# Optimization experiments

Hardware: AMD Instinct MI355X
Metric: run time of the kernel (lower is better)

## Reference

```python
import jax, jax.numpy as jnp
import numpy as np

N_NODES = 100000


def setup_inputs() -> dict:
    key = jax.random.key(0)
    ks = jax.random.split(key, 7)
    input_dim, hidden_dim = 64, 64
    x = jax.random.normal(ks[0], (N_NODES, input_dim), dtype=jnp.float32)
    edge_index = jax.random.randint(ks[1], (2, 1600000), 0, N_NODES, dtype=jnp.int64)
    weights = jax.random.uniform(ks[2], (N_NODES,), dtype=jnp.float32)
    # MLP params: Linear(input_dim->hidden), ReLU, Linear(hidden->hidden)
    s1 = 1.0 / np.sqrt(input_dim)
    s2 = 1.0 / np.sqrt(hidden_dim)
    W1 = jax.random.uniform(ks[3], (input_dim, hidden_dim), minval=-s1, maxval=s1, dtype=jnp.float32)
    b1 = jax.random.uniform(ks[4], (hidden_dim,), minval=-s1, maxval=s1, dtype=jnp.float32)
    W2 = jax.random.uniform(ks[5], (hidden_dim, hidden_dim), minval=-s2, maxval=s2, dtype=jnp.float32)
    b2 = jax.random.uniform(ks[6], (hidden_dim,), minval=-s2, maxval=s2, dtype=jnp.float32)
    return {"x": x, "edge_index": edge_index, "weights": weights,
            "W1": W1, "b1": b1, "W2": W2, "b2": b2}


def reference(x, edge_index, weights, W1, b1, W2, b2):
    src, dst = edge_index[0], edge_index[1]
    # GINConv (eps=0): h_i = MLP(x_i + sum_{j->i} x_j)
    agg = jax.ops.segment_sum(x[src], dst, num_segments=N_NODES)  # [N, d]
    h = agg + x
    h = jnp.maximum(h @ W1 + b1, 0.0)
    h = h @ W2 + b2                                                # [N, hidden]
    # per-node weighting then sum over nodes -> [1, 1, hidden]
    out = jnp.sum(h * weights[:, None], axis=0)
    return out[None, None, :]
```

## Files before the change

kernel.cpp:

```cpp
#include <hip/hip_runtime.h>
#include <hip/hip_bf16.h>

#define N_NODES 100000
#define N_EDGES 1600000
#define DIM 64
#define NB1 391
#define NGROUPS (N_NODES / 4)
#define NBLK_GM 1536
#define CSTRIDE 100096
#define E4 (N_EDGES / 4)
#define E4BLK 1563

#define OFF_COUNTS8 0
#define OFF_SOUT    800768
#define OFF_TOT     800848
#define OFF_OFFSETS 900944
#define OFF_BSUMS   1000960
#define OFF_CSR     1001472
#define OFF_RANK8   2601472
#define OFF_Y16     3001472

__device__ __forceinline__ float blo(unsigned u) { return __uint_as_float(u << 16); }
__device__ __forceinline__ float bhi(unsigned u) { return __uint_as_float(u & 0xffff0000u); }

__global__ __launch_bounds__(256) void convert_hist_kernel(
    const float* __restrict__ x, unsigned* __restrict__ y,
    const int* __restrict__ dst, int* __restrict__ counts8,
    unsigned* __restrict__ rank8)
{
    int i = blockIdx.x * 256 + threadIdx.x;
    if (i < N_NODES * DIM / 4) {
        float4 v = ((const float4*)x)[i];
        __hip_bfloat162 p0 = __float22bfloat162_rn(make_float2(v.x, v.y));
        __hip_bfloat162 p1 = __float22bfloat162_rn(make_float2(v.z, v.w));
        uint2 o;
        o.x = *reinterpret_cast<unsigned*>(&p0);
        o.y = *reinterpret_cast<unsigned*>(&p1);
        ((uint2*)y)[i] = o;
    }
    if (i < E4) {
        int4 d = ((const int4*)dst)[i];
        int* cnt = counts8 + (blockIdx.x & 7) * CSTRIDE;
        unsigned r0 = (unsigned)atomicAdd(&cnt[d.x], 1);
        unsigned r1 = (unsigned)atomicAdd(&cnt[d.y], 1);
        unsigned r2 = (unsigned)atomicAdd(&cnt[d.z], 1);
        unsigned r3 = (unsigned)atomicAdd(&cnt[d.w], 1);
        rank8[i] = r0 | (r1 << 8) | (r2 << 16) | (r3 << 24);
    }
}

__global__ __launch_bounds__(256) void colsum_blocksum_kernel(
    int* __restrict__ counts8, int* __restrict__ tot, int* __restrict__ bsums)
{
    __shared__ int s[256];
    int t = threadIdx.x;
    int idx = blockIdx.x * 256 + t;
    int run = 0;
    if (idx < N_NODES) {
        #pragma unroll
        for (int k = 0; k < 8; ++k) {
            int v = counts8[k * CSTRIDE + idx];
            counts8[k * CSTRIDE + idx] = run;
            run += v;
        }
        tot[idx] = run;
    }
    s[t] = (idx < N_NODES) ? run : 0;
    __syncthreads();
    for (int d = 128; d > 0; d >>= 1) {
        if (t < d) s[t] += s[t + d];
        __syncthreads();
    }
    if (t == 0) bsums[blockIdx.x] = s[0];
}

__global__ __launch_bounds__(512) void scanblocks_kernel(int* __restrict__ bsums)
{
    __shared__ int s[512];
    int t = threadIdx.x;
    int v = (t < NB1) ? bsums[t] : 0;
    s[t] = v;
    __syncthreads();
    for (int d = 1; d < 512; d <<= 1) {
        int add = (t >= d) ? s[t - d] : 0;
        __syncthreads();
        s[t] += add;
        __syncthreads();
    }
    if (t < NB1) bsums[t] = (t == 0) ? 0 : s[t - 1];
}

__global__ __launch_bounds__(256) void offsets_kernel(
    const int* __restrict__ tot, const int* __restrict__ bsums,
    int* __restrict__ offsets, int* __restrict__ counts8)
{
    __shared__ int s[256];
    int t = threadIdx.x;
    int idx = blockIdx.x * 256 + t;
    int c = (idx < N_NODES) ? tot[idx] : 0;
    s[t] = c;
    __syncthreads();
    for (int d = 1; d < 256; d <<= 1) {
        int add = (t >= d) ? s[t - d] : 0;
        __syncthreads();
        s[t] += add;
        __syncthreads();
    }
    int excl = (t == 0) ? 0 : s[t - 1];
    int off = bsums[blockIdx.x] + excl;
    if (idx < N_NODES) {
        offsets[idx] = off;
        #pragma unroll
        for (int k = 0; k < 8; ++k)
            counts8[k * CSTRIDE + idx] += off;
    }
    if (idx == 0) offsets[N_NODES] = N_EDGES;
}

__global__ __launch_bounds__(256) void fill_kernel(
    const int* __restrict__ src, const int* __restrict__ dst,
    const int* __restrict__ counts8, const unsigned* __restrict__ rank8,
    int* __restrict__ csr)
{
    int e4 = blockIdx.x * 256 + threadIdx.x;
    if (e4 < E4) {
        int4 s = ((const int4*)src)[e4];
        int4 d = ((const int4*)dst)[e4];
        unsigned rp = rank8[e4];
        const int* base = counts8 + (((unsigned)e4 >> 8) & 7) * CSTRIDE;
        int p0 = base[d.x] + (int)(rp & 255u);
        int p1 = base[d.y] + (int)((rp >> 8) & 255u);
        int p2 = base[d.z] + (int)((rp >> 16) & 255u);
        int p3 = base[d.w] + (int)((rp >> 24) & 255u);
        csr[p0] = s.x;
        csr[p1] = s.y;
        csr[p2] = s.z;
        csr[p3] = s.w;
    }
}

__global__ __launch_bounds__(256) void gather_mlp_kernel(
    const float* __restrict__ x,
    const unsigned* __restrict__ y16,
    const int* __restrict__ offsets,
    const int* __restrict__ csr,
    const float* __restrict__ weights,
    const float* __restrict__ W1,
    const float* __restrict__ b1,
    float* __restrict__ sout)
{
    __shared__ float W1s[DIM * DIM];
    __shared__ float vbuf[4][4][DIM];
    __shared__ float sred[4][DIM];

    const int tid  = threadIdx.x;
    const int lane = tid & 63;
    const int wave = tid >> 6;
    const int slot = lane >> 3;
    const int h    = lane & 7;

    for (int i = tid; i < DIM * DIM; i += 256) W1s[i] = W1[i];
    __syncthreads();

    const float bias = b1[lane];
    float sacc  = 0.f;
    float swacc = 0.f;

    const uint4* yrows = (const uint4*)y16;

    for (int g = blockIdx.x * 4 + wave; g < NGROUPS; g += NBLK_GM * 4) {
        const int i0 = g * 4;

        int off_l = offsets[i0 + (lane < 5 ? lane : 4)];
        int bg[4], dd[4];
        #pragma unroll
        for (int n = 0; n < 4; ++n) {
            int b = __builtin_amdgcn_readfirstlane(__shfl(off_l, n));
            int e = __builtin_amdgcn_readfirstlane(__shfl(off_l, n + 1));
            bg[n] = b; dd[n] = e - b;
        }

        int idx[4];
        float selfv[4];
        #pragma unroll
        for (int n = 0; n < 4; ++n)
            idx[n] = (lane < dd[n]) ? csr[bg[n] + lane] : 0;
        #pragma unroll
        for (int n = 0; n < 4; ++n)
            selfv[n] = x[(size_t)(i0 + n) * DIM + lane];

        uint4 r[4][3];
        #pragma unroll
        for (int n = 0; n < 4; ++n) {
            #pragma unroll
            for (int c = 0; c < 3; ++c) {
                r[n][c] = make_uint4(0u, 0u, 0u, 0u);
                if (c * 8 < dd[n]) {
                    const int e = c * 8 + slot;
                    const int s = __shfl(idx[n], e);
                    uint4 rr = yrows[(size_t)s * 8 + h];
                    if (e < dd[n]) r[n][c] = rr;
                }
            }
        }

        #pragma unroll
        for (int n = 0; n < 4; ++n) {
            float a0 = 0.f, a1 = 0.f, a2 = 0.f, a3 = 0.f;
            float a4 = 0.f, a5 = 0.f, a6 = 0.f, a7 = 0.f;
            #pragma unroll
            for (int c = 0; c < 3; ++c) {
                uint4 rr = r[n][c];
                a0 += blo(rr.x); a1 += bhi(rr.x);
                a2 += blo(rr.y); a3 += bhi(rr.y);
                a4 += blo(rr.z); a5 += bhi(rr.z);
                a6 += blo(rr.w); a7 += bhi(rr.w);
            }
            if (dd[n] > 24) {
                const int dcap = dd[n] <= 64 ? dd[n] : 64;
                for (int c = 3; c * 8 < dcap; ++c) {
                    const int e = c * 8 + slot;
                    const int s = __shfl(idx[n], e < 64 ? e : 0);
                    if (e < dcap) {
                        uint4 rr = yrows[(size_t)s * 8 + h];
                        a0 += blo(rr.x); a1 += bhi(rr.x);
                        a2 += blo(rr.y); a3 += bhi(rr.y);
                        a4 += blo(rr.z); a5 += bhi(rr.z);
                        a6 += blo(rr.w); a7 += bhi(rr.w);
                    }
                }
                if (dd[n] > 64) {
                    for (int jj = bg[n] + 64; jj < bg[n] + dd[n]; ++jj) {
                        const int s = csr[jj];
                        if (slot == 0) {
                            uint4 rr = yrows[(size_t)s * 8 + h];
                            a0 += blo(rr.x); a1 += bhi(rr.x);
                            a2 += blo(rr.y); a3 += bhi(rr.y);
                            a4 += blo(rr.z); a5 += bhi(rr.z);
                            a6 += blo(rr.w); a7 += bhi(rr.w);
                        }
                    }
                }
            }
            #pragma unroll
            for (int m = 8; m <= 32; m <<= 1) {
                a0 += __shfl_xor(a0, m); a1 += __shfl_xor(a1, m);
                a2 += __shfl_xor(a2, m); a3 += __shfl_xor(a3, m);
                a4 += __shfl_xor(a4, m); a5 += __shfl_xor(a5, m);
                a6 += __shfl_xor(a6, m); a7 += __shfl_xor(a7, m);
            }
            if (lane < 8) {
                *(float4*)&vbuf[wave][n][lane * 8]     = make_float4(a0, a1, a2, a3);
                *(float4*)&vbuf[wave][n][lane * 8 + 4] = make_float4(a4, a5, a6, a7);
            }
            vbuf[wave][n][lane] += selfv[n];
        }

        float a0 = bias, a1 = bias, a2 = bias, a3 = bias;
        #pragma unroll
        for (int k = 0; k < DIM; k += 4) {
            float4 q0 = *(const float4*)&vbuf[wave][0][k];
            float4 q1 = *(const float4*)&vbuf[wave][1][k];
            float4 q2 = *(const float4*)&vbuf[wave][2][k];
            float4 q3 = *(const float4*)&vbuf[wave][3][k];
            float w0 = W1s[(k + 0) * DIM + lane];
            float w1 = W1s[(k + 1) * DIM + lane];
            float w2 = W1s[(k + 2) * DIM + lane];
            float w3 = W1s[(k + 3) * DIM + lane];
            a0 = fmaf(q0.x, w0, a0); a0 = fmaf(q0.y, w1, a0);
            a0 = fmaf(q0.z, w2, a0); a0 = fmaf(q0.w, w3, a0);
            a1 = fmaf(q1.x, w0, a1); a1 = fmaf(q1.y, w1, a1);
            a1 = fmaf(q1.z, w2, a1); a1 = fmaf(q1.w, w3, a1);
            a2 = fmaf(q2.x, w0, a2); a2 = fmaf(q2.y, w1, a2);
            a2 = fmaf(q2.z, w2, a2); a2 = fmaf(q2.w, w3, a2);
            a3 = fmaf(q3.x, w0, a3); a3 = fmaf(q3.y, w1, a3);
            a3 = fmaf(q3.z, w2, a3); a3 = fmaf(q3.w, w3, a3);
        }

        const float wt0 = weights[i0 + 0];
        const float wt1 = weights[i0 + 1];
        const float wt2 = weights[i0 + 2];
        const float wt3 = weights[i0 + 3];
        sacc = fmaf(fmaxf(a0, 0.f), wt0, sacc);
        sacc = fmaf(fmaxf(a1, 0.f), wt1, sacc);
        sacc = fmaf(fmaxf(a2, 0.f), wt2, sacc);
        sacc = fmaf(fmaxf(a3, 0.f), wt3, sacc);
        if (lane == 0) swacc += wt0 + wt1 + wt2 + wt3;
    }

    sred[wave][lane] = sacc;
    __syncthreads();
    if (wave == 0) {
        float t = sred[0][lane] + sred[1][lane] + sred[2][lane] + sred[3][lane];
        atomicAdd(&sout[lane], t);
    }
    if (lane == 0) atomicAdd(&sout[DIM], swacc);
}

__global__ void finalize_kernel(
    const float* __restrict__ sout,
    const float* __restrict__ W2,
    const float* __restrict__ b2,
    float* __restrict__ out)
{
    const int j = threadIdx.x;
    const float sw = sout[DIM];
    float acc = sw * b2[j];
    #pragma unroll
    for (int k = 0; k < DIM; ++k)
        acc = fmaf(sout[k], W2[k * DIM + j], acc);
    out[j] = acc;
}

extern "C" void kernel_launch(void* const* d_in, const int* in_sizes, int n_in,
                              void* d_out, int out_size, void* d_ws, size_t ws_size,
                              hipStream_t stream)
{
    const float* x       = (const float*)d_in[0];
    const int*   ei      = (const int*)d_in[1];
    const float* weights = (const float*)d_in[2];
    const float* W1      = (const float*)d_in[3];
    const float* b1      = (const float*)d_in[4];
    const float* W2      = (const float*)d_in[5];
    const float* b2      = (const float*)d_in[6];
    float* out = (float*)d_out;

    const int* src = ei;
    const int* dst = ei + N_EDGES;

    int*      wsI     = (int*)d_ws;
    int*      counts8 = wsI + OFF_COUNTS8;
    float*    soutF   = (float*)(wsI + OFF_SOUT);
    int*      tot     = wsI + OFF_TOT;
    int*      offsets = wsI + OFF_OFFSETS;
    int*      bsums   = wsI + OFF_BSUMS;
    int*      csr     = wsI + OFF_CSR;
    unsigned* rank8   = (unsigned*)(wsI + OFF_RANK8);
    unsigned* y16     = (unsigned*)(wsI + OFF_Y16);

    hipMemsetAsync(d_ws, 0, (size_t)(OFF_SOUT + 80) * sizeof(int), stream);

    convert_hist_kernel  <<<(N_NODES * DIM / 4 + 255) / 256, 256, 0, stream>>>(x, y16, dst, counts8, rank8);
    colsum_blocksum_kernel<<<NB1,   256, 0, stream>>>(counts8, tot, bsums);
    scanblocks_kernel    <<<1,      512, 0, stream>>>(bsums);
    offsets_kernel       <<<NB1,    256, 0, stream>>>(tot, bsums, offsets, counts8);
    fill_kernel          <<<E4BLK,  256, 0, stream>>>(src, dst, counts8, rank8, csr);
    gather_mlp_kernel    <<<NBLK_GM, 256, 0, stream>>>(x, y16, offsets, csr, weights, W1, b1, soutF);
    finalize_kernel      <<<1,       64, 0, stream>>>(soutF, W2, b2, out);
}
```

Baseline: 296.8 us.

## Compress gathered features to 8-bit, fuse scan and finalize kernels

Neighbor feature rows are now stored as 8-bit truncated fp16 (sign, exponent, top mantissa bits) instead of bf16, halving the bytes each gathered row costs. The gather is reorganized around 16 edges per pass at 4 lanes per row. The separate block-scan kernel is folded into the offsets kernel, where each block sums its preceding block totals. The finalize kernel is merged into the gather kernel through a last-block-done atomic counter. This cuts memory traffic and two launches, but the much coarser encoding adds large quantization error to the aggregation, and occupancy is hinted at 5 blocks.

```diff
diff --git a/kernel.cpp b/kernel.cpp
--- a/kernel.cpp
+++ b/kernel.cpp
@@ -1,5 +1,5 @@
 #include <hip/hip_runtime.h>
-#include <hip/hip_bf16.h>
+#include <hip/hip_fp16.h>
 
 #define N_NODES 100000
 #define N_EDGES 1600000
@@ -18,25 +18,38 @@
 #define OFF_BSUMS   1000960
 #define OFF_CSR     1001472
 #define OFF_RANK8   2601472
-#define OFF_Y16     3001472
-
-__device__ __forceinline__ float blo(unsigned u) { return __uint_as_float(u << 16); }
-__device__ __forceinline__ float bhi(unsigned u) { return __uint_as_float(u & 0xffff0000u); }
+#define OFF_Y8      3001472
+
+__device__ __forceinline__ unsigned enc8(float f) {
+    __half h = __float2half_rn(f);
+    unsigned hb = (unsigned)__half_as_ushort(h);
+    return ((hb + 0x80u) >> 8) & 0xFFu;
+}
+
+__device__ __forceinline__ void unpack16(uint4 rr, float* acc) {
+    const unsigned w[4] = {rr.x, rr.y, rr.z, rr.w};
+    #pragma unroll
+    for (int wi = 0; wi < 4; ++wi) {
+        unsigned he = (w[wi] & 0x00FF00FFu) << 8;
+        unsigned ho =  w[wi] & 0xFF00FF00u;
+        float2 fe = __half22float2(*(__half2*)&he);
+        float2 fo = __half22float2(*(__half2*)&ho);
+        acc[wi * 4 + 0] += fe.x;
+        acc[wi * 4 + 1] += fo.x;
+        acc[wi * 4 + 2] += fe.y;
+        acc[wi * 4 + 3] += fo.y;
+    }
+}
 
 __global__ __launch_bounds__(256) void convert_hist_kernel(
-    const float* __restrict__ x, unsigned* __restrict__ y,
+    const float* __restrict__ x, unsigned* __restrict__ y8,
     const int* __restrict__ dst, int* __restrict__ counts8,
     unsigned* __restrict__ rank8)
 {
     int i = blockIdx.x * 256 + threadIdx.x;
     if (i < N_NODES * DIM / 4) {
         float4 v = ((const float4*)x)[i];
-        __hip_bfloat162 p0 = __float22bfloat162_rn(make_float2(v.x, v.y));
-        __hip_bfloat162 p1 = __float22bfloat162_rn(make_float2(v.z, v.w));
-        uint2 o;
-        o.x = *reinterpret_cast<unsigned*>(&p0);
-        o.y = *reinterpret_cast<unsigned*>(&p1);
-        ((uint2*)y)[i] = o;
+        y8[i] = enc8(v.x) | (enc8(v.y) << 8) | (enc8(v.z) << 16) | (enc8(v.w) << 24);
     }
     if (i < E4) {
         int4 d = ((const int4*)dst)[i];
@@ -74,29 +87,30 @@
     if (t == 0) bsums[blockIdx.x] = s[0];
 }
 
-__global__ __launch_bounds__(512) void scanblocks_kernel(int* __restrict__ bsums)
-{
-    __shared__ int s[512];
-    int t = threadIdx.x;
-    int v = (t < NB1) ? bsums[t] : 0;
-    s[t] = v;
-    __syncthreads();
-    for (int d = 1; d < 512; d <<= 1) {
-        int add = (t >= d) ? s[t - d] : 0;
-        __syncthreads();
-        s[t] += add;
-        __syncthreads();
-    }
-    if (t < NB1) bsums[t] = (t == 0) ? 0 : s[t - 1];
-}
-
 __global__ __launch_bounds__(256) void offsets_kernel(
     const int* __restrict__ tot, const int* __restrict__ bsums,
     int* __restrict__ offsets, int* __restrict__ counts8)
 {
     __shared__ int s[256];
-    int t = threadIdx.x;
-    int idx = blockIdx.x * 256 + t;
+    __shared__ int base_sh;
+    const int t = threadIdx.x;
+    const int bid = blockIdx.x;
+
+    int contrib = 0;
+    if (t < bid) contrib += bsums[t];
+    if (t + 256 < bid) contrib += bsums[t + 256];
+    s[t] = contrib;
+    __syncthreads();
+    for (int d = 128; d > 0; d >>= 1) {
+        if (t < d) s[t] += s[t + d];
+        __syncthreads();
+    }
+    if (t == 0) base_sh = s[0];
+    __syncthreads();
+    const int base = base_sh;
+    __syncthreads();
+
+    int idx = bid * 256 + t;
     int c = (idx < N_NODES) ? tot[idx] : 0;
     s[t] = c;
     __syncthreads();
@@ -107,7 +121,7 @@
         __syncthreads();
     }
     int excl = (t == 0) ? 0 : s[t - 1];
-    int off = bsums[blockIdx.x] + excl;
+    int off = base + excl;
     if (idx < N_NODES) {
         offsets[idx] = off;
         #pragma unroll
@@ -128,37 +142,39 @@
         int4 d = ((const int4*)dst)[e4];
         unsigned rp = rank8[e4];
         const int* base = counts8 + (((unsigned)e4 >> 8) & 7) * CSTRIDE;
-        int p0 = base[d.x] + (int)(rp & 255u);
-        int p1 = base[d.y] + (int)((rp >> 8) & 255u);
-        int p2 = base[d.z] + (int)((rp >> 16) & 255u);
-        int p3 = base[d.w] + (int)((rp >> 24) & 255u);
-        csr[p0] = s.x;
-        csr[p1] = s.y;
-        csr[p2] = s.z;
-        csr[p3] = s.w;
-    }
-}
-
-__global__ __launch_bounds__(256) void gather_mlp_kernel(
+        csr[base[d.x] + (int)(rp & 255u)]         = s.x;
+        csr[base[d.y] + (int)((rp >> 8) & 255u)]  = s.y;
+        csr[base[d.z] + (int)((rp >> 16) & 255u)] = s.z;
+        csr[base[d.w] + (int)((rp >> 24) & 255u)] = s.w;
+    }
+}
+
+__global__ __launch_bounds__(256, 5) void gather_mlp_kernel(
     const float* __restrict__ x,
-    const unsigned* __restrict__ y16,
+    const unsigned* __restrict__ y8,
     const int* __restrict__ offsets,
     const int* __restrict__ csr,
     const float* __restrict__ weights,
     const float* __restrict__ W1,
     const float* __restrict__ b1,
-    float* __restrict__ sout)
+    const float* __restrict__ W2,
+    const float* __restrict__ b2,
+    float* __restrict__ sout,
+    int* __restrict__ done,
+    float* __restrict__ out)
 {
     __shared__ float W1s[DIM * DIM];
     __shared__ float vbuf[4][4][DIM];
     __shared__ float sred[4][DIM];
+    __shared__ int islast;
 
     const int tid  = threadIdx.x;
     const int lane = tid & 63;
     const int wave = tid >> 6;
-    const int slot = lane >> 3;
-    const int h    = lane & 7;
-
+    const int slot16 = lane >> 2;
+    const int q      = lane & 3;
+
+    if (tid == 0) islast = 0;
     for (int i = tid; i < DIM * DIM; i += 256) W1s[i] = W1[i];
     __syncthreads();
 
@@ -166,7 +182,7 @@
     float sacc  = 0.f;
     float swacc = 0.f;
 
-    const uint4* yrows = (const uint4*)y16;
+    const uint4* yrows = (const uint4*)y8;
 
     for (int g = blockIdx.x * 4 + wave; g < NGROUPS; g += NBLK_GM * 4) {
         const int i0 = g * 4;
@@ -180,25 +196,25 @@
             bg[n] = b; dd[n] = e - b;
         }
 
-        int idx[4];
+        int idxv[4];
         float selfv[4];
         #pragma unroll
         for (int n = 0; n < 4; ++n)
-            idx[n] = (lane < dd[n]) ? csr[bg[n] + lane] : 0;
+            idxv[n] = (lane < dd[n]) ? csr[bg[n] + lane] : 0;
         #pragma unroll
         for (int n = 0; n < 4; ++n)
             selfv[n] = x[(size_t)(i0 + n) * DIM + lane];
 
-        uint4 r[4][3];
+        uint4 r[4][2];
         #pragma unroll
         for (int n = 0; n < 4; ++n) {
             #pragma unroll
-            for (int c = 0; c < 3; ++c) {
+            for (int c = 0; c < 2; ++c) {
                 r[n][c] = make_uint4(0u, 0u, 0u, 0u);
-                if (c * 8 < dd[n]) {
-                    const int e = c * 8 + slot;
-                    const int s = __shfl(idx[n], e);
-                    uint4 rr = yrows[(size_t)s * 8 + h];
+                if (c * 16 < dd[n]) {
+                    const int e = c * 16 + slot16;
+                    const int sI = __shfl(idxv[n], e);
+                    uint4 rr = yrows[(size_t)sI * 4 + q];
                     if (e < dd[n]) r[n][c] = rr;
                 }
             }
@@ -206,52 +222,53 @@
 
         #pragma unroll
         for (int n = 0; n < 4; ++n) {
-            float a0 = 0.f, a1 = 0.f, a2 = 0.f, a3 = 0.f;
-            float a4 = 0.f, a5 = 0.f, a6 = 0.f, a7 = 0.f;
+            float acc[16];
             #pragma unroll
-            for (int c = 0; c < 3; ++c) {
-                uint4 rr = r[n][c];
-                a0 += blo(rr.x); a1 += bhi(rr.x);
-                a2 += blo(rr.y); a3 += bhi(rr.y);
-                a4 += blo(rr.z); a5 += bhi(rr.z);
-                a6 += blo(rr.w); a7 += bhi(rr.w);
-            }
-            if (dd[n] > 24) {
+            for (int i = 0; i < 16; ++i) acc[i] = 0.f;
+            unpack16(r[n][0], acc);
+            unpack16(r[n][1], acc);
+
+            if (dd[n] > 32) {
                 const int dcap = dd[n] <= 64 ? dd[n] : 64;
-                for (int c = 3; c * 8 < dcap; ++c) {
-                    const int e = c * 8 + slot;
-                    const int s = __shfl(idx[n], e < 64 ? e : 0);
-                    if (e < dcap) {
-                        uint4 rr = yrows[(size_t)s * 8 + h];
-                        a0 += blo(rr.x); a1 += bhi(rr.x);
-                        a2 += blo(rr.y); a3 += bhi(rr.y);
-                        a4 += blo(rr.z); a5 += bhi(rr.z);
-                        a6 += blo(rr.w); a7 += bhi(rr.w);
+                #pragma unroll
+                for (int c = 2; c < 4; ++c) {
+                    if (c * 16 < dcap) {
+                        const int e = c * 16 + slot16;
+                        const int sI = __shfl(idxv[n], e);
+                        if (e < dcap) {
+                            uint4 rr = yrows[(size_t)sI * 4 + q];
+                            unpack16(rr, acc);
+                        }
                     }
                 }
                 if (dd[n] > 64) {
-                    for (int jj = bg[n] + 64; jj < bg[n] + dd[n]; ++jj) {
-                        const int s = csr[jj];
-                        if (slot == 0) {
-                            uint4 rr = yrows[(size_t)s * 8 + h];
-                            a0 += blo(rr.x); a1 += bhi(rr.x);
-                            a2 += blo(rr.y); a3 += bhi(rr.y);
-                            a4 += blo(rr.z); a5 += bhi(rr.z);
-                            a6 += blo(rr.w); a7 += bhi(rr.w);
+                    for (int b0i = 64; b0i < dd[n]; b0i += 64) {
+                        int rem = dd[n] - b0i; if (rem > 64) rem = 64;
+                        int idx2 = (lane < rem) ? csr[bg[n] + b0i + lane] : 0;
+                        for (int c = 0; c * 16 < rem; ++c) {
+                            const int e = c * 16 + slot16;
+                            const int sI = __shfl(idx2, e);
+                            if (e < rem) {
+                                uint4 rr = yrows[(size_t)sI * 4 + q];
+                                unpack16(rr, acc);
+                            }
                         }
                     }
                 }
             }
+
             #pragma unroll
-            for (int m = 8; m <= 32; m <<= 1) {
-                a0 += __shfl_xor(a0, m); a1 += __shfl_xor(a1, m);
-                a2 += __shfl_xor(a2, m); a3 += __shfl_xor(a3, m);
-                a4 += __shfl_xor(a4, m); a5 += __shfl_xor(a5, m);
-                a6 += __shfl_xor(a6, m); a7 += __shfl_xor(a7, m);
+            for (int m = 4; m <= 32; m <<= 1) {
+                #pragma unroll
+                for (int i = 0; i < 16; ++i)
+                    acc[i] += __shfl_xor(acc[i], m);
             }
-            if (lane < 8) {
-                *(float4*)&vbuf[wave][n][lane * 8]     = make_float4(a0, a1, a2, a3);
-                *(float4*)&vbuf[wave][n][lane * 8 + 4] = make_float4(a4, a5, a6, a7);
+            if (lane < 4) {
+                #pragma unroll
+                for (int ii = 0; ii < 4; ++ii)
+                    *(float4*)&vbuf[wave][n][lane * 16 + ii * 4] =
+                        make_float4(acc[ii * 4 + 0], acc[ii * 4 + 1],
+                                    acc[ii * 4 + 2], acc[ii * 4 + 3]);
             }
             vbuf[wave][n][lane] += selfv[n];
         }
@@ -295,21 +312,24 @@
         atomicAdd(&sout[lane], t);
     }
     if (lane == 0) atomicAdd(&sout[DIM], swacc);
-}
-
-__global__ void finalize_kernel(
-    const float* __restrict__ sout,
-    const float* __restrict__ W2,
-    const float* __restrict__ b2,
-    float* __restrict__ out)
-{
-    const int j = threadIdx.x;
-    const float sw = sout[DIM];
-    float acc = sw * b2[j];
-    #pragma unroll
-    for (int k = 0; k < DIM; ++k)
-        acc = fmaf(sout[k], W2[k * DIM + j], acc);
-    out[j] = acc;
+
+    __syncthreads();
+    if (tid == 0) {
+        __threadfence();
+        int prev = atomicAdd(done, 1);
+        islast = (prev == NBLK_GM - 1) ? 1 : 0;
+    }
+    __syncthreads();
+    if (islast && tid < DIM) {
+        __threadfence();
+        const int j = tid;
+        const float sw = sout[DIM];
+        float acc = sw * b2[j];
+        #pragma unroll
+        for (int k = 0; k < DIM; ++k)
+            acc = fmaf(sout[k], W2[k * DIM + j], acc);
+        out[j] = acc;
+    }
 }
 
 extern "C" void kernel_launch(void* const* d_in, const int* in_sizes, int n_in,
@@ -331,20 +351,19 @@
     int*      wsI     = (int*)d_ws;
     int*      counts8 = wsI + OFF_COUNTS8;
     float*    soutF   = (float*)(wsI + OFF_SOUT);
+    int*      done    = wsI + OFF_SOUT + 72;
     int*      tot     = wsI + OFF_TOT;
     int*      offsets = wsI + OFF_OFFSETS;
     int*      bsums   = wsI + OFF_BSUMS;
     int*      csr     = wsI + OFF_CSR;
     unsigned* rank8   = (unsigned*)(wsI + OFF_RANK8);
-    unsigned* y16     = (unsigned*)(wsI + OFF_Y16);
+    unsigned* y8      = (unsigned*)(wsI + OFF_Y8);
 
     hipMemsetAsync(d_ws, 0, (size_t)(OFF_SOUT + 80) * sizeof(int), stream);
 
-    convert_hist_kernel  <<<(N_NODES * DIM / 4 + 255) / 256, 256, 0, stream>>>(x, y16, dst, counts8, rank8);
-    colsum_blocksum_kernel<<<NB1,   256, 0, stream>>>(counts8, tot, bsums);
-    scanblocks_kernel    <<<1,      512, 0, stream>>>(bsums);
-    offsets_kernel       <<<NB1,    256, 0, stream>>>(tot, bsums, offsets, counts8);
-    fill_kernel          <<<E4BLK,  256, 0, stream>>>(src, dst, counts8, rank8, csr);
-    gather_mlp_kernel    <<<NBLK_GM, 256, 0, stream>>>(x, y16, offsets, csr, weights, W1, b1, soutF);
-    finalize_kernel      <<<1,       64, 0, stream>>>(soutF, W2, b2, out);
-}
+    convert_hist_kernel   <<<(N_NODES * DIM / 4 + 255) / 256, 256, 0, stream>>>(x, y8, dst, counts8, rank8);
+    colsum_blocksum_kernel<<<NB1,    256, 0, stream>>>(counts8, tot, bsums);
+    offsets_kernel        <<<NB1,    256, 0, stream>>>(tot, bsums, offsets, counts8);
+    fill_kernel           <<<E4BLK,  256, 0, stream>>>(src, dst, counts8, rank8, csr);
+    gather_mlp_kernel     <<<NBLK_GM, 256, 0, stream>>>(x, y8, offsets, csr, weights, W1, b1, W2, b2, soutF, done, out);
+}
```

After: 359.9 us. 1.21x slower.

## Prefetch next group's CSR metadata in gather loop and fold block scan into offsets

Applied to the files above, without the earlier changes.

The gather-MLP loop now loads the next group's offsets, neighbor indices and self features while the current group's row gathers are in flight, a software pipeline meant to hide dependent-load latency. The separate single-block scan kernel is removed: each offsets block reduces the preceding block sums itself, which saves one launch at the cost of redundant reads. The gather grid also grows from 1536 to 1792 blocks. Prefetching raises register pressure, which may cut occupancy.

```diff
diff --git a/kernel.cpp b/kernel.cpp
--- a/kernel.cpp
+++ b/kernel.cpp
@@ -6,7 +6,7 @@
 #define DIM 64
 #define NB1 391
 #define NGROUPS (N_NODES / 4)
-#define NBLK_GM 1536
+#define NBLK_GM 1792
 #define CSTRIDE 100096
 #define E4 (N_EDGES / 4)
 #define E4BLK 1563
@@ -74,29 +74,30 @@
     if (t == 0) bsums[blockIdx.x] = s[0];
 }
 
-__global__ __launch_bounds__(512) void scanblocks_kernel(int* __restrict__ bsums)
-{
-    __shared__ int s[512];
-    int t = threadIdx.x;
-    int v = (t < NB1) ? bsums[t] : 0;
-    s[t] = v;
-    __syncthreads();
-    for (int d = 1; d < 512; d <<= 1) {
-        int add = (t >= d) ? s[t - d] : 0;
-        __syncthreads();
-        s[t] += add;
-        __syncthreads();
-    }
-    if (t < NB1) bsums[t] = (t == 0) ? 0 : s[t - 1];
-}
-
 __global__ __launch_bounds__(256) void offsets_kernel(
     const int* __restrict__ tot, const int* __restrict__ bsums,
     int* __restrict__ offsets, int* __restrict__ counts8)
 {
     __shared__ int s[256];
-    int t = threadIdx.x;
-    int idx = blockIdx.x * 256 + t;
+    __shared__ int base_sh;
+    const int t = threadIdx.x;
+    const int bid = blockIdx.x;
+
+    int contrib = 0;
+    if (t < bid) contrib += bsums[t];
+    if (t + 256 < bid) contrib += bsums[t + 256];
+    s[t] = contrib;
+    __syncthreads();
+    for (int d = 128; d > 0; d >>= 1) {
+        if (t < d) s[t] += s[t + d];
+        __syncthreads();
+    }
+    if (t == 0) base_sh = s[0];
+    __syncthreads();
+    const int base = base_sh;
+    __syncthreads();
+
+    int idx = bid * 256 + t;
     int c = (idx < N_NODES) ? tot[idx] : 0;
     s[t] = c;
     __syncthreads();
@@ -107,7 +108,7 @@
         __syncthreads();
     }
     int excl = (t == 0) ? 0 : s[t - 1];
-    int off = bsums[blockIdx.x] + excl;
+    int off = base + excl;
     if (idx < N_NODES) {
         offsets[idx] = off;
         #pragma unroll
@@ -128,14 +129,10 @@
         int4 d = ((const int4*)dst)[e4];
         unsigned rp = rank8[e4];
         const int* base = counts8 + (((unsigned)e4 >> 8) & 7) * CSTRIDE;
-        int p0 = base[d.x] + (int)(rp & 255u);
-        int p1 = base[d.y] + (int)((rp >> 8) & 255u);
-        int p2 = base[d.z] + (int)((rp >> 16) & 255u);
-        int p3 = base[d.w] + (int)((rp >> 24) & 255u);
-        csr[p0] = s.x;
-        csr[p1] = s.y;
-        csr[p2] = s.z;
-        csr[p3] = s.w;
+        csr[base[d.x] + (int)(rp & 255u)]         = s.x;
+        csr[base[d.y] + (int)((rp >> 8) & 255u)]  = s.y;
+        csr[base[d.z] + (int)((rp >> 16) & 255u)] = s.z;
+        csr[base[d.w] + (int)((rp >> 24) & 255u)] = s.w;
     }
 }
 
@@ -167,27 +164,30 @@
     float swacc = 0.f;
 
     const uint4* yrows = (const uint4*)y16;
-
-    for (int g = blockIdx.x * 4 + wave; g < NGROUPS; g += NBLK_GM * 4) {
-        const int i0 = g * 4;
-
-        int off_l = offsets[i0 + (lane < 5 ? lane : 4)];
-        int bg[4], dd[4];
+    const int oidx = (lane < 5 ? lane : 4);
+
+    int g = blockIdx.x * 4 + wave;
+    int bg[4], dd[4], idxv[4];
+    float selfv[4];
+
+    if (g < NGROUPS) {
+        int off_l = offsets[g * 4 + oidx];
         #pragma unroll
         for (int n = 0; n < 4; ++n) {
             int b = __builtin_amdgcn_readfirstlane(__shfl(off_l, n));
             int e = __builtin_amdgcn_readfirstlane(__shfl(off_l, n + 1));
             bg[n] = b; dd[n] = e - b;
         }
-
-        int idx[4];
-        float selfv[4];
         #pragma unroll
         for (int n = 0; n < 4; ++n)
-            idx[n] = (lane < dd[n]) ? csr[bg[n] + lane] : 0;
+            idxv[n] = (lane < dd[n]) ? csr[bg[n] + lane] : 0;
         #pragma unroll
         for (int n = 0; n < 4; ++n)
-            selfv[n] = x[(size_t)(i0 + n) * DIM + lane];
+            selfv[n] = x[(size_t)(g * 4 + n) * DIM + lane];
+    }
+
+    while (g < NGROUPS) {
+        const int i0 = g * 4;
 
         uint4 r[4][3];
         #pragma unroll
@@ -197,11 +197,30 @@
                 r[n][c] = make_uint4(0u, 0u, 0u, 0u);
                 if (c * 8 < dd[n]) {
                     const int e = c * 8 + slot;
-                    const int s = __shfl(idx[n], e);
+                    const int s = __shfl(idxv[n], e);
                     uint4 rr = yrows[(size_t)s * 8 + h];
                     if (e < dd[n]) r[n][c] = rr;
                 }
             }
+        }
+
+        const int gn = g + NBLK_GM * 4;
+        int bgn[4], ddn[4], idxn[4];
+        float selfn[4];
+        if (gn < NGROUPS) {
+            int off_ln = offsets[gn * 4 + oidx];
+            #pragma unroll
+            for (int n = 0; n < 4; ++n) {
+                int b = __builtin_amdgcn_readfirstlane(__shfl(off_ln, n));
+                int e = __builtin_amdgcn_readfirstlane(__shfl(off_ln, n + 1));
+                bgn[n] = b; ddn[n] = e - b;
+            }
+            #pragma unroll
+            for (int n = 0; n < 4; ++n)
+                idxn[n] = (lane < ddn[n]) ? csr[bgn[n] + lane] : 0;
+            #pragma unroll
+            for (int n = 0; n < 4; ++n)
+                selfn[n] = x[(size_t)(gn * 4 + n) * DIM + lane];
         }
 
         #pragma unroll
@@ -220,7 +239,7 @@
                 const int dcap = dd[n] <= 64 ? dd[n] : 64;
                 for (int c = 3; c * 8 < dcap; ++c) {
                     const int e = c * 8 + slot;
-                    const int s = __shfl(idx[n], e < 64 ? e : 0);
+                    const int s = __shfl(idxv[n], e < 64 ? e : 0);
                     if (e < dcap) {
                         uint4 rr = yrows[(size_t)s * 8 + h];
                         a0 += blo(rr.x); a1 += bhi(rr.x);
@@ -286,6 +305,13 @@
         sacc = fmaf(fmaxf(a2, 0.f), wt2, sacc);
         sacc = fmaf(fmaxf(a3, 0.f), wt3, sacc);
         if (lane == 0) swacc += wt0 + wt1 + wt2 + wt3;
+
+        g = gn;
+        #pragma unroll
+        for (int n = 0; n < 4; ++n) {
+            bg[n] = bgn[n]; dd[n] = ddn[n];
+            idxv[n] = idxn[n]; selfv[n] = selfn[n];
+        }
     }
 
     sred[wave][lane] = sacc;
@@ -340,11 +366,10 @@
 
     hipMemsetAsync(d_ws, 0, (size_t)(OFF_SOUT + 80) * sizeof(int), stream);
 
-    convert_hist_kernel  <<<(N_NODES * DIM / 4 + 255) / 256, 256, 0, stream>>>(x, y16, dst, counts8, rank8);
-    colsum_blocksum_kernel<<<NB1,   256, 0, stream>>>(counts8, tot, bsums);
-    scanblocks_kernel    <<<1,      512, 0, stream>>>(bsums);
-    offsets_kernel       <<<NB1,    256, 0, stream>>>(tot, bsums, offsets, counts8);
-    fill_kernel          <<<E4BLK,  256, 0, stream>>>(src, dst, counts8, rank8, csr);
-    gather_mlp_kernel    <<<NBLK_GM, 256, 0, stream>>>(x, y16, offsets, csr, weights, W1, b1, soutF);
-    finalize_kernel      <<<1,       64, 0, stream>>>(soutF, W2, b2, out);
-}
+    convert_hist_kernel   <<<(N_NODES * DIM / 4 + 255) / 256, 256, 0, stream>>>(x, y16, dst, counts8, rank8);
+    colsum_blocksum_kernel<<<NB1,    256, 0, stream>>>(counts8, tot, bsums);
+    offsets_kernel        <<<NB1,    256, 0, stream>>>(tot, bsums, offsets, counts8);
+    fill_kernel           <<<E4BLK,  256, 0, stream>>>(src, dst, counts8, rank8, csr);
+    gather_mlp_kernel     <<<NBLK_GM, 256, 0, stream>>>(x, y16, offsets, csr, weights, W1, b1, soutF);
+    finalize_kernel       <<<1,       64, 0, stream>>>(soutF, W2, b2, out);
+}
```

Result: slower. 305.6 us (+3.0%).
